# Kernel tuning notes

Hardware: AMD Instinct MI355X
Metric: run time of the kernel (lower is better)

The kernel has to match this reference:

```python
import jax, jax.numpy as jnp
import numpy as np

B, S, D, H, F, E, K = 2, 2048, 1024, 16, 4096, 8, 2
DH = D // H
EPS = 1e-6  # RMSNorm eps (torch nn.RMSNorm default ~ fp32 machine eps; 1e-6 used here)


def _rmsnorm(x, w):
    return x * jax.lax.rsqrt(jnp.mean(x * x, axis=-1, keepdims=True) + EPS) * w


def setup_inputs() -> dict:
    key = jax.random.key(0)
    ks = jax.random.split(key, 16)
    std = 0.02
    return {
        "x": jax.random.normal(ks[0], (B, S, D), jnp.float32),
        "norm1_w": jnp.ones((D,), jnp.float32),
        "norm2_w": jnp.ones((D,), jnp.float32),
        "w_qkv": jax.random.normal(ks[1], (D, 3 * D), jnp.float32) * std,
        "b_qkv": jnp.zeros((3 * D,), jnp.float32),
        "w_o": jax.random.normal(ks[2], (D, D), jnp.float32) * std,
        "b_o": jnp.zeros((D,), jnp.float32),
        "router_w": jax.random.normal(ks[3], (D, E), jnp.float32) * std,
        "router_b": jnp.zeros((E,), jnp.float32),
        "w1": jax.random.normal(ks[4], (E, D, F), jnp.float32) * std,
        "b1": jnp.zeros((E, F), jnp.float32),
        "w2": jax.random.normal(ks[5], (E, F, D), jnp.float32) * std,
        "b2": jnp.zeros((E, D), jnp.float32),
    }


def reference(x, norm1_w, norm2_w, w_qkv, b_qkv, w_o, b_o,
              router_w, router_b, w1, b1, w2, b2):
    # ---- pre-norm causal multi-head attention ----
    h = _rmsnorm(x, norm1_w)
    qkv = h @ w_qkv + b_qkv                                  # [B,S,3D]
    q, k, v = jnp.split(qkv, 3, axis=-1)
    q = q.reshape(B, S, H, DH).transpose(0, 2, 1, 3)         # [B,H,S,DH]
    k = k.reshape(B, S, H, DH).transpose(0, 2, 1, 3)
    v = v.reshape(B, S, H, DH).transpose(0, 2, 1, 3)
    scores = jnp.einsum('bhqd,bhkd->bhqk', q, k) / jnp.sqrt(jnp.asarray(DH, x.dtype))
    causal = jnp.tril(jnp.ones((S, S), bool))
    scores = jnp.where(causal, scores, jnp.asarray(-1e9, x.dtype))
    attn = jax.nn.softmax(scores, axis=-1)
    ao = jnp.einsum('bhqk,bhkd->bhqd', attn, v).transpose(0, 2, 1, 3).reshape(B, S, D)
    x = x + (ao @ w_o + b_o)

    # ---- pre-norm top-k MoE feed-forward ----
    h2 = _rmsnorm(x, norm2_w)
    t = h2.reshape(-1, D)                                    # [T,D], T=B*S
    logits = t @ router_w + router_b                         # [T,E]
    probs = jax.nn.softmax(logits, axis=-1)
    topv, topi = jax.lax.top_k(probs, K)                     # [T,K]
    gates_k = topv / jnp.sum(topv, axis=-1, keepdims=True)   # renormalized top-k gates
    oh = jax.nn.one_hot(topi, E, dtype=x.dtype)              # [T,K,E]
    gates = jnp.einsum('tke,tk->te', oh, gates_k)            # dense gates, zero off top-k

    out = jnp.zeros_like(t)
    for e in range(E):                                       # fixed small expert loop
        he = jax.nn.gelu(t @ w1[e] + b1[e], approximate=False)
        ye = he @ w2[e] + b2[e]
        out = out + gates[:, e:e + 1] * ye

    # load-balancing aux loss: E * sum_e f_e * P_e
    f = jnp.mean(jnp.sum(oh, axis=1), axis=0)                # fraction routed to each expert
    P = jnp.mean(probs, axis=0)                              # mean router prob per expert
    aux_loss = jnp.asarray(E, x.dtype) * jnp.sum(f * P)

    x = x + out.reshape(B, S, D)
    return (x, aux_loss)
```

## Files before the change

### kernel.cpp

```cpp
#include <hip/hip_runtime.h>
#include <math.h>

#define TB 2
#define TS 2048
#define TD 1024
#define TH 16
#define TDH 64
#define TF 4096
#define TE 8
#define TT 4096
#define PSTR (TB*TH*TS*TDH)

typedef __attribute__((ext_vector_type(8))) __bf16 bf16x8;
typedef __attribute__((ext_vector_type(4))) float f32x4;
typedef __attribute__((ext_vector_type(8))) short short8;
typedef __attribute__((ext_vector_type(4))) unsigned short ushort4v;
typedef __attribute__((ext_vector_type(4))) float fvec4;

__device__ inline unsigned short f2bf(float f) {
  union { float f; unsigned int u; } v; v.f = f;
  unsigned int u = v.u;
  unsigned int r = (u + 0x7FFFu + ((u >> 16) & 1u)) >> 16;
  return (unsigned short)r;
}
__device__ inline float bf2f(unsigned short h) {
  union { unsigned int u; float f; } v; v.u = ((unsigned int)h) << 16; return v.f;
}
__device__ inline void split2(float x, unsigned short& h, unsigned short& m) {
  h = f2bf(x);
  m = f2bf(x - bf2f(h));
}

__device__ inline f32x4 mfma_bf16(short8 a, short8 b, f32x4 c) {
  return __builtin_amdgcn_mfma_f32_16x16x32_bf16(
      __builtin_bit_cast(bf16x8, a), __builtin_bit_cast(bf16x8, b), c, 0, 0, 0);
}

__device__ inline void gload16(const void* g, void* l) {
  __builtin_amdgcn_global_load_lds(
      (const __attribute__((address_space(1))) void*)g,
      (__attribute__((address_space(3))) void*)l, 16, 0, 0);
}

__device__ inline float gelu_f(float v) {
  float ax = fabsf(v) * 0.70710678118654752f;
  float t = __builtin_amdgcn_rcpf(1.0f + 0.3275911f * ax);
  float poly = ((((1.061405429f * t - 1.453152027f) * t + 1.421413741f) * t
                 - 0.284496736f) * t + 0.254829592f) * t;
  float er = 1.0f - poly * __expf(-ax * ax);
  er = copysignf(er, v);
  return 0.5f * v * (1.0f + er);
}

__global__ __launch_bounds__(256)
void tcvt_kernel(const float* __restrict__ In, unsigned short* __restrict__ Out,
                 int R, int C) {
  __shared__ float tile[32][33];
  In  += (size_t)blockIdx.z * R * C;
  Out += (size_t)blockIdx.z * R * C;
  int c0 = blockIdx.x * 32, r0 = blockIdx.y * 32;
  int tx = threadIdx.x & 31, ty = threadIdx.x >> 5;
#pragma unroll
  for (int i = 0; i < 4; ++i)
    tile[ty + 8*i][tx] = In[(size_t)(r0 + ty + 8*i) * C + c0 + tx];
  __syncthreads();
#pragma unroll
  for (int i = 0; i < 4; ++i)
    Out[(size_t)(c0 + ty + 8*i) * R + r0 + tx] = f2bf(tile[tx][ty + 8*i]);
}

__global__ __launch_bounds__(256)
void tcvt_split_kernel(const float* __restrict__ In,
                       unsigned short* __restrict__ O0,
                       unsigned short* __restrict__ O1, int R, int C) {
  __shared__ float tile[32][33];
  int c0 = blockIdx.x * 32, r0 = blockIdx.y * 32;
  int tx = threadIdx.x & 31, ty = threadIdx.x >> 5;
#pragma unroll
  for (int i = 0; i < 4; ++i)
    tile[ty + 8*i][tx] = In[(size_t)(r0 + ty + 8*i) * C + c0 + tx];
  __syncthreads();
#pragma unroll
  for (int i = 0; i < 4; ++i) {
    float v = tile[tx][ty + 8*i];
    unsigned short h, m; split2(v, h, m);
    size_t idx = (size_t)(c0 + ty + 8*i) * R + r0 + tx;
    O0[idx] = h; O1[idx] = m;
  }
}

__global__ __launch_bounds__(256)
void rmsnorm_kernel(const float* __restrict__ X, const float* __restrict__ W,
                    unsigned short* __restrict__ O) {
  int row = blockIdx.x;
  int tid = threadIdx.x;
  int lane = tid & 63, wave = tid >> 6;
  const float* xr = X + (size_t)row * TD;
  fvec4 v = *(const fvec4*)(xr + tid * 4);
  float ss = v[0]*v[0] + v[1]*v[1] + v[2]*v[2] + v[3]*v[3];
#pragma unroll
  for (int msk = 1; msk < 64; msk <<= 1) ss += __shfl_xor(ss, msk);
  __shared__ float red[4];
  if (lane == 0) red[wave] = ss;
  __syncthreads();
  ss = red[0] + red[1] + red[2] + red[3];
  float rs = rsqrtf(ss * (1.0f / TD) + 1e-6f);
  fvec4 wv = *(const fvec4*)(W + tid * 4);
  ushort4v o;
#pragma unroll
  for (int j = 0; j < 4; ++j) o[j] = f2bf(v[j] * rs * wv[j]);
  *(ushort4v*)(O + (size_t)row * TD + tid * 4) = o;
}

__global__ __launch_bounds__(256)
void rmsnorm_split_kernel(const float* __restrict__ X, const float* __restrict__ W,
                          unsigned short* __restrict__ O0,
                          unsigned short* __restrict__ O1) {
  int row = blockIdx.x;
  int tid = threadIdx.x;
  int lane = tid & 63, wave = tid >> 6;
  const float* xr = X + (size_t)row * TD;
  fvec4 v = *(const fvec4*)(xr + tid * 4);
  float ss = v[0]*v[0] + v[1]*v[1] + v[2]*v[2] + v[3]*v[3];
#pragma unroll
  for (int msk = 1; msk < 64; msk <<= 1) ss += __shfl_xor(ss, msk);
  __shared__ float red[4];
  if (lane == 0) red[wave] = ss;
  __syncthreads();
  ss = red[0] + red[1] + red[2] + red[3];
  float rs = rsqrtf(ss * (1.0f / TD) + 1e-6f);
  fvec4 wv = *(const fvec4*)(W + tid * 4);
  ushort4v o0, o1;
#pragma unroll
  for (int j = 0; j < 4; ++j) {
    unsigned short h, m; split2(v[j] * rs * wv[j], h, m);
    o0[j] = h; o1[j] = m;
  }
  size_t idx = (size_t)row * TD + tid * 4;
  *(ushort4v*)(O0 + idx) = o0;
  *(ushort4v*)(O1 + idx) = o1;
}

template<int MODE>
__global__ __launch_bounds__(256)
void gemm2(const unsigned short* __restrict__ A0,
           const unsigned short* __restrict__ A1,
           const unsigned short* __restrict__ B0,
           const unsigned short* __restrict__ B1,
           const float* __restrict__ bias, int Kd,
           float* __restrict__ outF, const float* __restrict__ resid,
           unsigned short* __restrict__ S0,
           unsigned short* __restrict__ S1) {
  __shared__ __align__(16) unsigned short As0[2][4096], As1[2][4096];
  __shared__ __align__(16) unsigned short Bs0[2][4096], Bs1[2][4096];
  const int tid = threadIdx.x;
  const int lane = tid & 63;
  const int w = tid >> 6;
  const int wr = w >> 1, wc = w & 1;
  const int g = lane >> 4;
  const int l15 = lane & 15;
  const int m0 = blockIdx.y * 128;
  const int n0 = blockIdx.x * 128;

  const int c_swz = (lane & 3) ^ ((lane >> 3) & 3);
  const unsigned short *a0p[2], *a1p[2], *b0p[2], *b1p[2];
  int ldsrow[2];
#pragma unroll
  for (int j = 0; j < 2; ++j) {
    int r16 = w * 2 + j;
    int r = r16 * 16 + (lane >> 2);
    a0p[j] = A0 + (size_t)(m0 + r) * Kd + c_swz * 8;
    a1p[j] = A1 + (size_t)(m0 + r) * Kd + c_swz * 8;
    b0p[j] = B0 + (size_t)(n0 + r) * Kd + c_swz * 8;
    b1p[j] = B1 + (size_t)(n0 + r) * Kd + c_swz * 8;
    ldsrow[j] = r16 * 512;
  }

#define G2_STAGE(p, koff)                              \
  {                                                    \
    _Pragma("unroll")                                  \
    for (int j = 0; j < 2; ++j) {                      \
      gload16(a0p[j] + (koff), &As0[p][ldsrow[j]]);    \
      gload16(a1p[j] + (koff), &As1[p][ldsrow[j]]);    \
      gload16(b0p[j] + (koff), &Bs0[p][ldsrow[j]]);    \
      gload16(b1p[j] + (koff), &Bs1[p][ldsrow[j]]);    \
    }                                                  \
  }

  f32x4 acc[4][4] = {};
  const int nt = Kd >> 5;

  G2_STAGE(0, 0);
  for (int t = 0; t < nt; ++t) {
    const int p = t & 1;
    if (t + 1 < nt) {
      G2_STAGE(p ^ 1, (t + 1) * 32);
      asm volatile("s_waitcnt vmcnt(8)" ::: "memory");
    } else {
      asm volatile("s_waitcnt vmcnt(0)" ::: "memory");
    }
    __builtin_amdgcn_s_barrier();

    short8 a0f[4], a1f[4], b0f[4], b1f[4];
#pragma unroll
    for (int mi = 0; mi < 4; ++mi) {
      int row = wr * 64 + mi * 16 + l15;
      int off = (row * 64 + g * 16) ^ (((row >> 1) & 3) << 4);
      a0f[mi] = *(const short8*)((const char*)As0[p] + off);
      a1f[mi] = *(const short8*)((const char*)As1[p] + off);
    }
#pragma unroll
    for (int ni = 0; ni < 4; ++ni) {
      int row = wc * 64 + ni * 16 + l15;
      int off = (row * 64 + g * 16) ^ (((row >> 1) & 3) << 4);
      b0f[ni] = *(const short8*)((const char*)Bs0[p] + off);
      b1f[ni] = *(const short8*)((const char*)Bs1[p] + off);
    }
#pragma unroll
    for (int mi = 0; mi < 4; ++mi)
#pragma unroll
      for (int ni = 0; ni < 4; ++ni) {
        f32x4 tacc = acc[mi][ni];
        tacc = mfma_bf16(a0f[mi], b0f[ni], tacc);
        tacc = mfma_bf16(a0f[mi], b1f[ni], tacc);
        tacc = mfma_bf16(a1f[mi], b0f[ni], tacc);
        acc[mi][ni] = tacc;
      }
    __builtin_amdgcn_s_barrier();
  }
#undef G2_STAGE

#pragma unroll
  for (int mi = 0; mi < 4; ++mi) {
#pragma unroll
    for (int ni = 0; ni < 4; ++ni) {
      int n = n0 + wc * 64 + ni * 16 + l15;
      float bv = bias[n];
      if (MODE == 0) {
        int part = n >> 10, d = n & 1023, hh = d >> 6, dh = d & 63;
        int s0r = m0 + wr * 64 + mi * 16 + g * 4;
        int b = s0r >> 11, s_ = s0r & 2047;
        int bh = b * TH + hh;
        if (part < 2) {
          size_t base = (size_t)part * PSTR + (size_t)bh * (TS * TDH) + (size_t)s_ * TDH + dh;
#pragma unroll
          for (int r = 0; r < 4; ++r) {
            unsigned short h, m; split2(acc[mi][ni][r] + bv, h, m);
            size_t idx = base + (size_t)r * TDH;
            S0[idx] = h; S1[idx] = m;
          }
        } else {
          ushort4v o0, o1;
#pragma unroll
          for (int r = 0; r < 4; ++r) {
            unsigned short h, m; split2(acc[mi][ni][r] + bv, h, m);
            o0[r] = h; o1[r] = m;
          }
          size_t idx = 2 * (size_t)PSTR + (size_t)bh * (TS * TDH) + (size_t)dh * TS + s_;
          *(ushort4v*)(S0 + idx) = o0;
          *(ushort4v*)(S1 + idx) = o1;
        }
      } else {
#pragma unroll
        for (int r = 0; r < 4; ++r) {
          int m = m0 + wr * 64 + mi * 16 + g * 4 + r;
          size_t idx = (size_t)m * TD + n;
          outF[idx] = acc[mi][ni][r] + bv + resid[idx];
        }
      }
    }
  }
}

__global__ __launch_bounds__(512, 4)
void attn2_kernel(const unsigned short* __restrict__ S0,
                  const unsigned short* __restrict__ S1,
                  unsigned short* __restrict__ A0,
                  unsigned short* __restrict__ A1) {
  __shared__ __align__(16) char Kt0[8192], Kt1[8192];
  __shared__ __align__(16) char Vt0[8192], Vt1[8192];
  __shared__ __align__(16) char Pt0[16384], Pt1[16384];

  const int tid = threadIdx.x;
  const int lane = tid & 63;
  const int wave = tid >> 6;
  const int g = lane >> 4, l15 = lane & 15;

  const int bh = blockIdx.y;
  const int b = bh >> 4, hh = bh & 15;

  const size_t qbase = (size_t)bh * TS * TDH;
  const size_t kbase = (size_t)PSTR + qbase;
  const size_t vbase = 2 * (size_t)PSTR + qbase;

  for (int half = 0; half < 2; ++half) {
    const int qtb = half ? (15 - (int)blockIdx.x) : (int)blockIdx.x;
    const int qlo = qtb * 128 + wave * 16;

    short8 aq0[2], aq1[2];
#pragma unroll
    for (int c = 0; c < 2; ++c) {
      size_t qo = qbase + (size_t)(qlo + l15) * TDH + c * 32 + g * 8;
      aq0[c] = *(const short8*)(S0 + qo);
      aq1[c] = *(const short8*)(S1 + qo);
    }

    f32x4 accv[4] = {};
    float m_[4] = {-1e30f, -1e30f, -1e30f, -1e30f};
    float l_[4] = {0.f, 0.f, 0.f, 0.f};

    const int ktmax = 2 * qtb + 1;
    for (int kt = 0; kt <= ktmax; ++kt) {
      __syncthreads();
      {
        int row = tid >> 3, ch = tid & 7;
        int off = (row * 128 + ch * 16) ^ ((row & 7) << 4);
        size_t kg = kbase + (size_t)(kt * 64 + row) * TDH + ch * 8;
        *(short8*)(Kt0 + off) = *(const short8*)(S0 + kg);
        *(short8*)(Kt1 + off) = *(const short8*)(S1 + kg);
        size_t vg = vbase + (size_t)row * TS + kt * 64 + ch * 8;
        *(short8*)(Vt0 + off) = *(const short8*)(S0 + vg);
        *(short8*)(Vt1 + off) = *(const short8*)(S1 + vg);
      }
      __syncthreads();

      if (kt * 64 > qlo + 15) continue;
      const bool needmask = (kt * 64 + 63 > qlo);

      f32x4 sf[4] = {};
#pragma unroll
      for (int kb = 0; kb < 4; ++kb) {
#pragma unroll
        for (int c = 0; c < 2; ++c) {
          int krow = kb * 16 + l15;
          int off = (krow * 128 + (c * 32 + g * 8) * 2) ^ ((krow & 7) << 4);
          short8 bk0 = *(const short8*)(Kt0 + off);
          short8 bk1 = *(const short8*)(Kt1 + off);
          f32x4 t = sf[kb];
          t = mfma_bf16(aq0[c], bk0, t);
          t = mfma_bf16(aq0[c], bk1, t);
          t = mfma_bf16(aq1[c], bk0, t);
          sf[kb] = t;
        }
      }

      float pv[4][4];
#pragma unroll
      for (int r = 0; r < 4; ++r) {
        float s0 = sf[0][r] * 0.125f, s1 = sf[1][r] * 0.125f;
        float s2 = sf[2][r] * 0.125f, s3 = sf[3][r] * 0.125f;
        if (needmask) {
          int qg = qlo + g * 4 + r;
          int k0g = kt * 64 + l15;
          if (k0g      > qg) s0 = -1e30f;
          if (k0g + 16 > qg) s1 = -1e30f;
          if (k0g + 32 > qg) s2 = -1e30f;
          if (k0g + 48 > qg) s3 = -1e30f;
        }
        float mx = fmaxf(fmaxf(s0, s1), fmaxf(s2, s3));
#pragma unroll
        for (int msk = 1; msk < 16; msk <<= 1) mx = fmaxf(mx, __shfl_xor(mx, msk));
        float nm = fmaxf(m_[r], mx);
        float sc = __expf(m_[r] - nm);
        float p0 = __expf(s0 - nm), p1 = __expf(s1 - nm);
        float p2 = __expf(s2 - nm), p3 = __expf(s3 - nm);
        float rs = p0 + p1 + p2 + p3;
#pragma unroll
        for (int msk = 1; msk < 16; msk <<= 1) rs += __shfl_xor(rs, msk);
        m_[r] = nm;
        l_[r] = l_[r] * sc + rs;
#pragma unroll
        for (int dhb = 0; dhb < 4; ++dhb) accv[dhb][r] *= sc;
        pv[0][r] = p0; pv[1][r] = p1; pv[2][r] = p2; pv[3][r] = p3;
      }

      char* P0 = Pt0 + wave * 2048;
      char* P1 = Pt1 + wave * 2048;
#pragma unroll
      for (int kb = 0; kb < 4; ++kb) {
#pragma unroll
        for (int r = 0; r < 4; ++r) {
          int prow = g * 4 + r;
          int key = kb * 16 + l15;
          int off = (prow * 128 + key * 2) ^ ((prow & 7) << 4);
          unsigned short h, m; split2(pv[kb][r], h, m);
          *(unsigned short*)(P0 + off) = h;
          *(unsigned short*)(P1 + off) = m;
        }
      }
      short8 pa0[2], pa1[2];
#pragma unroll
      for (int c = 0; c < 2; ++c) {
        int off = (l15 * 128 + (c * 32 + g * 8) * 2) ^ ((l15 & 7) << 4);
        pa0[c] = *(const short8*)(P0 + off);
        pa1[c] = *(const short8*)(P1 + off);
      }
#pragma unroll
      for (int dhb = 0; dhb < 4; ++dhb) {
#pragma unroll
        for (int c = 0; c < 2; ++c) {
          int dh = dhb * 16 + l15;
          int off = (dh * 128 + (c * 32 + g * 8) * 2) ^ ((dh & 7) << 4);
          short8 bv0 = *(const short8*)(Vt0 + off);
          short8 bv1 = *(const short8*)(Vt1 + off);
          f32x4 t = accv[dhb];
          t = mfma_bf16(pa0[c], bv0, t);
          t = mfma_bf16(pa0[c], bv1, t);
          t = mfma_bf16(pa1[c], bv0, t);
          accv[dhb] = t;
        }
      }
    }

#pragma unroll
    for (int dhb = 0; dhb < 4; ++dhb) {
#pragma unroll
      for (int r = 0; r < 4; ++r) {
        int srow = qlo + g * 4 + r;
        int col = hh * 64 + dhb * 16 + l15;
        unsigned short h, m; split2(accv[dhb][r] / l_[r], h, m);
        size_t idx = ((size_t)(b * TS + srow)) * TD + col;
        A0[idx] = h; A1[idx] = m;
      }
    }
  }
}

__global__ __launch_bounds__(256)
void moe_gather_kernel(const unsigned short* __restrict__ h2,
                       const int* __restrict__ tperm,
                       unsigned short* __restrict__ h2p) {
  int slot = blockIdx.x;
  int t = tperm[slot];
  const ushort4v* src = (const ushort4v*)(h2 + (size_t)t * TD);
  ushort4v* dst = (ushort4v*)(h2p + (size_t)slot * TD);
  dst[threadIdx.x] = src[threadIdx.x];
}

__global__ __launch_bounds__(512)
void gemm_up8(const unsigned short* __restrict__ A,
              const unsigned short* __restrict__ Bt,
              const float* __restrict__ bias,
              int N, int Kd,
              unsigned short* __restrict__ outH,
              const int* __restrict__ seg_off,
              const int* __restrict__ seg_cnt) {
  __shared__ __align__(16) unsigned short As[2][256 * 64];
  __shared__ __align__(16) unsigned short Bs[2][256 * 64];

  const int tid = threadIdx.x;
  const int lane = tid & 63;
  const int w = tid >> 6;
  const int wm = w >> 2, wn = w & 3;
  const int g = lane >> 4;
  const int l15 = lane & 15;

  const int e = blockIdx.z;
  const int m0 = blockIdx.y * 256;
  const int n0 = blockIdx.x * 256;
  const int off = seg_off[e];
  const int Mrows = seg_cnt[e];
  if (m0 >= Mrows) return;
  Bt += (size_t)e * N * Kd;
  bias += (size_t)e * N;

  const int gc = (lane & 7) ^ ((lane >> 3) & 7);
  const unsigned short* aptr[4];
  const unsigned short* bptr[4];
#pragma unroll
  for (int rnd = 0; rnd < 4; ++rnd) {
    int rl = rnd * 64 + w * 8 + (lane >> 3);
    int rc = (m0 + rl < Mrows) ? (m0 + rl) : (Mrows - 1);
    aptr[rnd] = A + (size_t)(off + rc) * Kd + gc * 8;
    bptr[rnd] = Bt + (size_t)(n0 + rl) * Kd + gc * 8;
  }

#define UP8_STAGE(p, koff)                                        \
  {                                                               \
    _Pragma("unroll")                                             \
    for (int rnd = 0; rnd < 4; ++rnd) {                           \
      gload16(aptr[rnd] + (koff), &As[p][(rnd * 64 + w * 8) * 64]); \
      gload16(bptr[rnd] + (koff), &Bs[p][(rnd * 64 + w * 8) * 64]); \
    }                                                             \
  }

  f32x4 acc[8][4] = {};
  const int nt = Kd >> 6;

  UP8_STAGE(0, 0);
  __syncthreads();

  for (int t = 0; t < nt; ++t) {
    const int p = t & 1;
    if (t + 1 < nt) UP8_STAGE(p ^ 1, (t + 1) * 64);

#pragma unroll
    for (int ph = 0; ph < 4; ++ph) {
      const int mh = ph >> 1, kk = ph & 1;
      short8 af[4], bfr[4];
#pragma unroll
      for (int q = 0; q < 4; ++q) {
        int row = wm * 128 + (mh * 4 + q) * 16 + l15;
        int o2 = row * 128 + ((((kk << 2) | g) ^ (row & 7)) << 4);
        af[q] = *(const short8*)((const char*)As[p] + o2);
      }
#pragma unroll
      for (int ni = 0; ni < 4; ++ni) {
        int row = wn * 64 + ni * 16 + l15;
        int o2 = row * 128 + ((((kk << 2) | g) ^ (row & 7)) << 4);
        bfr[ni] = *(const short8*)((const char*)Bs[p] + o2);
      }
#pragma unroll
      for (int q = 0; q < 4; ++q)
#pragma unroll
        for (int ni = 0; ni < 4; ++ni)
          acc[mh * 4 + q][ni] = mfma_bf16(af[q], bfr[ni], acc[mh * 4 + q][ni]);
    }
    __syncthreads();
  }
#undef UP8_STAGE

#pragma unroll
  for (int mi = 0; mi < 8; ++mi) {
#pragma unroll
    for (int ni = 0; ni < 4; ++ni) {
      int n = n0 + wn * 64 + ni * 16 + l15;
      float bv = bias[n];
#pragma unroll
      for (int r = 0; r < 4; ++r) {
        int mloc = m0 + wm * 128 + mi * 16 + g * 4 + r;
        if (mloc >= Mrows) continue;
        float val = acc[mi][ni][r] + bv;
        outH[(size_t)(off + mloc) * TF + n] = f2bf(gelu_f(val));
      }
    }
  }
}

__global__ __launch_bounds__(256)
void gemm_dn(const unsigned short* __restrict__ A,
             const unsigned short* __restrict__ Bt,
             const float* __restrict__ bias,
             int N, int Kd,
             float* __restrict__ ysl,
             const int* __restrict__ seg_off,
             const int* __restrict__ seg_cnt,
             const float* __restrict__ gate_perm) {
  __shared__ __align__(16) unsigned short As[2][4096];
  __shared__ __align__(16) unsigned short Bs[2][4096];

  const int tid = threadIdx.x;
  const int lane = tid & 63;
  const int w = tid >> 6;
  const int wr = w >> 1, wc = w & 1;
  const int g = lane >> 4;
  const int l15 = lane & 15;

  const int e = blockIdx.z;
  const int m0 = blockIdx.y * 128;
  const int n0 = blockIdx.x * 128;
  const int off = seg_off[e];
  const int Mrows = seg_cnt[e];
  if (m0 >= Mrows) return;
  Bt += (size_t)e * N * Kd;
  bias += (size_t)e * N;

  const int c_swz = (lane & 3) ^ ((lane >> 3) & 3);
  const unsigned short* aptr[2];
  const unsigned short* bptr[2];
  int ldsrow[2];
#pragma unroll
  for (int j = 0; j < 2; ++j) {
    int r16 = w * 2 + j;
    int r = r16 * 16 + (lane >> 2);
    int rc = (m0 + r < Mrows) ? (m0 + r) : (Mrows - 1);
    aptr[j] = A + (size_t)(off + rc) * Kd + c_swz * 8;
    bptr[j] = Bt + (size_t)(n0 + r) * Kd + c_swz * 8;
    ldsrow[j] = r16 * 512;
  }

#define GB_STAGE(p, koff)                           \
  {                                                 \
    _Pragma("unroll")                               \
    for (int j = 0; j < 2; ++j) {                   \
      gload16(aptr[j] + (koff), &As[p][ldsrow[j]]); \
      gload16(bptr[j] + (koff), &Bs[p][ldsrow[j]]); \
    }                                               \
  }

  f32x4 acc[4][4] = {};
  const int nt = Kd >> 5;

  GB_STAGE(0, 0);
  for (int t = 0; t < nt; ++t) {
    const int p = t & 1;
    if (t + 1 < nt) {
      GB_STAGE(p ^ 1, (t + 1) * 32);
      asm volatile("s_waitcnt vmcnt(4)" ::: "memory");
    } else {
      asm volatile("s_waitcnt vmcnt(0)" ::: "memory");
    }
    __builtin_amdgcn_s_barrier();

    short8 af[4], bfr[4];
#pragma unroll
    for (int mi = 0; mi < 4; ++mi) {
      int row = wr * 64 + mi * 16 + l15;
      int o2 = (row * 64 + g * 16) ^ (((row >> 1) & 3) << 4);
      af[mi] = *(const short8*)((const char*)As[p] + o2);
    }
#pragma unroll
    for (int ni = 0; ni < 4; ++ni) {
      int row = wc * 64 + ni * 16 + l15;
      int o2 = (row * 64 + g * 16) ^ (((row >> 1) & 3) << 4);
      bfr[ni] = *(const short8*)((const char*)Bs[p] + o2);
    }
#pragma unroll
    for (int mi = 0; mi < 4; ++mi)
#pragma unroll
      for (int ni = 0; ni < 4; ++ni)
        acc[mi][ni] = mfma_bf16(af[mi], bfr[ni], acc[mi][ni]);
    __builtin_amdgcn_s_barrier();
  }
#undef GB_STAGE

#pragma unroll
  for (int mi = 0; mi < 4; ++mi) {
#pragma unroll
    for (int ni = 0; ni < 4; ++ni) {
      int n = n0 + wc * 64 + ni * 16 + l15;
      float bv = bias[n];
#pragma unroll
      for (int r = 0; r < 4; ++r) {
        int mloc = m0 + wr * 64 + mi * 16 + g * 4 + r;
        if (mloc >= Mrows) continue;
        float val = acc[mi][ni][r] + bv;
        float gv = gate_perm[off + mloc];
        ysl[(size_t)(off + mloc) * TD + n] = gv * val;
      }
    }
  }
}

__global__ __launch_bounds__(256)
void moe_reduce_kernel(const float* __restrict__ ys, const int* __restrict__ tslot,
                       float* __restrict__ out) {
  int t = blockIdx.x;
  int d = threadIdx.x * 4;
  fvec4 a = *(const fvec4*)(ys + (size_t)tslot[t * 2] * TD + d);
  fvec4 b = *(const fvec4*)(ys + (size_t)tslot[t * 2 + 1] * TD + d);
  float* o = out + (size_t)t * TD + d;
  fvec4 c = *(const fvec4*)o;
#pragma unroll
  for (int j = 0; j < 4; ++j) c[j] += a[j] + b[j];
  *(fvec4*)o = c;
}

__global__ __launch_bounds__(256)
void router_kernel(const float* __restrict__ X1, const float* __restrict__ N2W,
                   const float* __restrict__ RW, const float* __restrict__ RB,
                   int* __restrict__ top_e, float* __restrict__ top_g,
                   int* __restrict__ counts, float* __restrict__ p_sum) {
  __shared__ float s_psum[TE];
  __shared__ int s_cnt[TE];
  if (threadIdx.x < TE) { s_psum[threadIdx.x] = 0.f; s_cnt[threadIdx.x] = 0; }
  __syncthreads();
  int lane = threadIdx.x & 63, wave = threadIdx.x >> 6;
  for (int it = 0; it < 16; ++it) {
    int t = (blockIdx.x * 4 + wave) * 16 + it;
    const float* xr = X1 + (size_t)t * TD;
    float vals[16]; float ss = 0.f;
#pragma unroll
    for (int i = 0; i < 16; ++i) { float xv = xr[i * 64 + lane]; vals[i] = xv; ss += xv * xv; }
#pragma unroll
    for (int msk = 1; msk < 64; msk <<= 1) ss += __shfl_xor(ss, msk);
    float rs = rsqrtf(ss * (1.0f / TD) + 1e-6f);
    float acc[TE] = {};
#pragma unroll
    for (int i = 0; i < 16; ++i) {
      int d = i * 64 + lane;
      float nv = vals[i] * rs * N2W[d];
      const float* rwp = RW + (size_t)d * TE;
#pragma unroll
      for (int e2 = 0; e2 < TE; ++e2) acc[e2] += nv * rwp[e2];
    }
#pragma unroll
    for (int msk = 1; msk < 64; msk <<= 1)
#pragma unroll
      for (int e2 = 0; e2 < TE; ++e2) acc[e2] += __shfl_xor(acc[e2], msk);
    if (lane == 0) {
      float lg[TE]; float mx = -1e30f;
      for (int e2 = 0; e2 < TE; ++e2) { lg[e2] = acc[e2] + RB[e2]; mx = fmaxf(mx, lg[e2]); }
      float sum = 0.f, pe[TE];
      for (int e2 = 0; e2 < TE; ++e2) { pe[e2] = expf(lg[e2] - mx); sum += pe[e2]; }
      float inv = 1.0f / sum;
      for (int e2 = 0; e2 < TE; ++e2) atomicAdd(&s_psum[e2], pe[e2] * inv);
      int i1 = 0;
      for (int e2 = 1; e2 < TE; ++e2) if (lg[e2] > lg[i1]) i1 = e2;
      int i2 = (i1 == 0) ? 1 : 0;
      for (int e2 = 0; e2 < TE; ++e2) if (e2 != i1 && lg[e2] > lg[i2]) i2 = e2;
      float g1 = pe[i1], g2 = pe[i2], gs = g1 + g2;
      top_e[t * 2] = i1; top_e[t * 2 + 1] = i2;
      top_g[t * 2] = g1 / gs; top_g[t * 2 + 1] = g2 / gs;
      atomicAdd(&s_cnt[i1], 1); atomicAdd(&s_cnt[i2], 1);
    }
  }
  __syncthreads();
  if (threadIdx.x < TE) {
    atomicAdd(&p_sum[threadIdx.x], s_psum[threadIdx.x]);
    atomicAdd(&counts[threadIdx.x], s_cnt[threadIdx.x]);
  }
}

__global__ void zero_meta_kernel(int* counts, float* p_sum) {
  int t = threadIdx.x;
  if (t < TE) { counts[t] = 0; p_sum[t] = 0.f; }
}

__global__ void offsets_kernel(const int* counts, int* offs, int* cursor) {
  if (threadIdx.x == 0) {
    int o = 0;
    for (int e2 = 0; e2 < TE; ++e2) { offs[e2] = o; o += counts[e2]; }
  }
  if (threadIdx.x < TE) cursor[threadIdx.x] = 0;
}

__global__ __launch_bounds__(256)
void fill_kernel(const int* __restrict__ top_e, const float* __restrict__ top_g,
                 const int* __restrict__ offs, int* __restrict__ cursor,
                 int* __restrict__ token_perm, float* __restrict__ gate_perm,
                 int* __restrict__ tslot) {
  __shared__ int s_cnt[TE], s_base[TE];
  if (threadIdx.x < TE) s_cnt[threadIdx.x] = 0;
  __syncthreads();
  int t = blockIdx.x * 256 + threadIdx.x;
  int e0 = top_e[t * 2], e1 = top_e[t * 2 + 1];
  int r0 = atomicAdd(&s_cnt[e0], 1);
  int r1 = atomicAdd(&s_cnt[e1], 1);
  __syncthreads();
  if (threadIdx.x < TE)
    s_base[threadIdx.x] = atomicAdd(&cursor[threadIdx.x], s_cnt[threadIdx.x]);
  __syncthreads();
  int p0 = offs[e0] + s_base[e0] + r0;
  int p1 = offs[e1] + s_base[e1] + r1;
  token_perm[p0] = t; gate_perm[p0] = top_g[t * 2];
  token_perm[p1] = t; gate_perm[p1] = top_g[t * 2 + 1];
  tslot[t * 2] = p0; tslot[t * 2 + 1] = p1;
}

__global__ void aux_kernel(const int* counts, const float* p_sum, float* outv) {
  if (threadIdx.x == 0) {
    float a = 0.f;
    for (int e2 = 0; e2 < TE; ++e2)
      a += ((float)counts[e2] / (float)TT) * (p_sum[e2] / (float)TT);
    outv[0] = (float)TE * a;
  }
}

extern "C" void kernel_launch(void* const* d_in, const int* in_sizes, int n_in,
                              void* d_out, int out_size, void* d_ws, size_t ws_size,
                              hipStream_t stream) {
  const float* x     = (const float*)d_in[0];
  const float* n1w   = (const float*)d_in[1];
  const float* n2w   = (const float*)d_in[2];
  const float* w_qkv = (const float*)d_in[3];
  const float* b_qkv = (const float*)d_in[4];
  const float* w_o   = (const float*)d_in[5];
  const float* b_o   = (const float*)d_in[6];
  const float* rw    = (const float*)d_in[7];
  const float* rb    = (const float*)d_in[8];
  const float* w1    = (const float*)d_in[9];
  const float* b1    = (const float*)d_in[10];
  const float* w2    = (const float*)d_in[11];
  const float* b2    = (const float*)d_in[12];
  float* out = (float*)d_out;
  char* ws = (char*)d_ws;

  size_t o = 0;
  auto give = [&](size_t bytes) -> char* {
    char* p = ws + o;
    o += (bytes + 255) & ~(size_t)255;
    return p;
  };
  unsigned short* w1T = (unsigned short*)give(8ull * 4096 * 1024 * 2);
  unsigned short* w2T = (unsigned short*)give(8ull * 1024 * 4096 * 2);
  unsigned short* wo0 = (unsigned short*)give(1024ull * 1024 * 2);
  unsigned short* wo1 = (unsigned short*)give(1024ull * 1024 * 2);
  unsigned short* h2  = (unsigned short*)give((size_t)TT * TD * 2);
  int*   counts = (int*)give(TE * 4);
  int*   cursor = (int*)give(TE * 4);
  int*   offs   = (int*)give(TE * 4);
  float* psum   = (float*)give(TE * 4);
  int*   top_e  = (int*)give(2ull * TT * 4);
  float* top_g  = (float*)give(2ull * TT * 4);
  int*   tperm  = (int*)give(2ull * TT * 4);
  float* gperm  = (float*)give(2ull * TT * 4);
  int*   tslot  = (int*)give(2ull * TT * 4);
  unsigned short* wq0 = (unsigned short*)give(3072ull * 1024 * 2);
  unsigned short* wq1 = (unsigned short*)give(3072ull * 1024 * 2);
  float* ys = (float*)give(2ull * TT * TD * 4);
  char* poolB = give(2ull * TT * TD * 2);
  unsigned short* h10 = (unsigned short*)poolB;
  unsigned short* h11 = (unsigned short*)(poolB + (size_t)TT * TD * 2);
  unsigned short* ao0 = h10; unsigned short* ao1 = h11;
  unsigned short* h2p = (unsigned short*)poolB;
  char* poolC = give(64ull * 1024 * 1024);
  unsigned short* qs0 = (unsigned short*)poolC;
  unsigned short* qs1 = (unsigned short*)(poolC + 3ull * PSTR * 2);
  unsigned short* he  = (unsigned short*)poolC;

  tcvt_split_kernel<<<dim3(96, 32, 1), 256, 0, stream>>>(w_qkv, wq0, wq1, 1024, 3072);
  tcvt_split_kernel<<<dim3(32, 32, 1), 256, 0, stream>>>(w_o, wo0, wo1, 1024, 1024);
  tcvt_kernel<<<dim3(128, 32, 8), 256, 0, stream>>>(w1, w1T, 1024, 4096);
  tcvt_kernel<<<dim3(32, 128, 8), 256, 0, stream>>>(w2, w2T, 4096, 1024);

  rmsnorm_split_kernel<<<dim3(TT), 256, 0, stream>>>(x, n1w, h10, h11);
  gemm2<0><<<dim3(24, 32, 1), 256, 0, stream>>>(
      h10, h11, wq0, wq1, b_qkv, 1024, nullptr, nullptr, qs0, qs1);
  attn2_kernel<<<dim3(8, 32, 1), 512, 0, stream>>>(qs0, qs1, ao0, ao1);
  gemm2<1><<<dim3(8, 32, 1), 256, 0, stream>>>(
      ao0, ao1, wo0, wo1, b_o, 1024, out, x, nullptr, nullptr);

  rmsnorm_kernel<<<dim3(TT), 256, 0, stream>>>(out, n2w, h2);
  zero_meta_kernel<<<dim3(1), 64, 0, stream>>>(counts, psum);
  router_kernel<<<dim3(64), 256, 0, stream>>>(out, n2w, rw, rb, top_e, top_g, counts, psum);
  offsets_kernel<<<dim3(1), 64, 0, stream>>>(counts, offs, cursor);
  fill_kernel<<<dim3(TT / 256), 256, 0, stream>>>(top_e, top_g, offs, cursor, tperm, gperm, tslot);
  moe_gather_kernel<<<dim3(2 * TT), 256, 0, stream>>>(h2, tperm, h2p);
  gemm_up8<<<dim3(16, 16, 8), 512, 0, stream>>>(
      h2p, w1T, b1, 4096, 1024, he, offs, counts);
  gemm_dn<<<dim3(8, 32, 8), 256, 0, stream>>>(
      he, w2T, b2, 1024, 4096, ys, offs, counts, gperm);
  moe_reduce_kernel<<<dim3(TT), 256, 0, stream>>>(ys, tslot, out);
  aux_kernel<<<dim3(1), 64, 0, stream>>>(counts, psum, out + (size_t)TT * TD);
}
```

Baseline: 756.9 us.

## Enlarge MoE down-proj GEMM tile to 256x128 with K=64 stages and counted waits

Replaces the 128x128, K=32 down-projection GEMM with a 512-thread, 256x128-tile kernel that uses K=64 stages and an XOR-swizzled LDS layout taken from the up-projection kernel. The larger tile halves the number of blocks and re-reads each B tile fewer times. It also swaps the up-projection kernel's __syncthreads for an explicit vmcnt wait plus barrier, so the prefetch for the next stage stays in flight during compute. In exchange it uses more LDS per block, and a single block covers more padded rows for small expert segments.

Result: slower. 828.2 us (+9.4%).

```diff
diff --git a/kernel.cpp b/kernel.cpp
--- a/kernel.cpp
+++ b/kernel.cpp
@@ -488,11 +488,15 @@
   const int nt = Kd >> 6;
 
   UP8_STAGE(0, 0);
-  __syncthreads();
-
   for (int t = 0; t < nt; ++t) {
     const int p = t & 1;
-    if (t + 1 < nt) UP8_STAGE(p ^ 1, (t + 1) * 64);
+    if (t + 1 < nt) {
+      UP8_STAGE(p ^ 1, (t + 1) * 64);
+      asm volatile("s_waitcnt vmcnt(8)" ::: "memory");
+    } else {
+      asm volatile("s_waitcnt vmcnt(0)" ::: "memory");
+    }
+    __builtin_amdgcn_s_barrier();
 
 #pragma unroll
     for (int ph = 0; ph < 4; ++ph) {
@@ -516,7 +520,7 @@
         for (int ni = 0; ni < 4; ++ni)
           acc[mh * 4 + q][ni] = mfma_bf16(af[q], bfr[ni], acc[mh * 4 + q][ni]);
     }
-    __syncthreads();
+    __builtin_amdgcn_s_barrier();
   }
 #undef UP8_STAGE
 
@@ -537,27 +541,27 @@
   }
 }
 
-__global__ __launch_bounds__(256)
-void gemm_dn(const unsigned short* __restrict__ A,
-             const unsigned short* __restrict__ Bt,
-             const float* __restrict__ bias,
-             int N, int Kd,
-             float* __restrict__ ysl,
-             const int* __restrict__ seg_off,
-             const int* __restrict__ seg_cnt,
-             const float* __restrict__ gate_perm) {
-  __shared__ __align__(16) unsigned short As[2][4096];
-  __shared__ __align__(16) unsigned short Bs[2][4096];
+__global__ __launch_bounds__(512)
+void gemm_dn8(const unsigned short* __restrict__ A,
+              const unsigned short* __restrict__ Bt,
+              const float* __restrict__ bias,
+              int N, int Kd,
+              float* __restrict__ ysl,
+              const int* __restrict__ seg_off,
+              const int* __restrict__ seg_cnt,
+              const float* __restrict__ gate_perm) {
+  __shared__ __align__(16) unsigned short As[2][256 * 64];
+  __shared__ __align__(16) unsigned short Bs[2][128 * 64];
 
   const int tid = threadIdx.x;
   const int lane = tid & 63;
   const int w = tid >> 6;
-  const int wr = w >> 1, wc = w & 1;
+  const int wm = w >> 1, wn = w & 1;
   const int g = lane >> 4;
   const int l15 = lane & 15;
 
   const int e = blockIdx.z;
-  const int m0 = blockIdx.y * 128;
+  const int m0 = blockIdx.y * 256;
   const int n0 = blockIdx.x * 128;
   const int off = seg_off[e];
   const int Mrows = seg_cnt[e];
@@ -565,74 +569,79 @@
   Bt += (size_t)e * N * Kd;
   bias += (size_t)e * N;
 
-  const int c_swz = (lane & 3) ^ ((lane >> 3) & 3);
-  const unsigned short* aptr[2];
+  const int gc = (lane & 7) ^ ((lane >> 3) & 7);
+  const unsigned short* aptr[4];
   const unsigned short* bptr[2];
-  int ldsrow[2];
+#pragma unroll
+  for (int rnd = 0; rnd < 4; ++rnd) {
+    int rl = rnd * 64 + w * 8 + (lane >> 3);
+    int rc = (m0 + rl < Mrows) ? (m0 + rl) : (Mrows - 1);
+    aptr[rnd] = A + (size_t)(off + rc) * Kd + gc * 8;
+  }
 #pragma unroll
   for (int j = 0; j < 2; ++j) {
-    int r16 = w * 2 + j;
-    int r = r16 * 16 + (lane >> 2);
-    int rc = (m0 + r < Mrows) ? (m0 + r) : (Mrows - 1);
-    aptr[j] = A + (size_t)(off + rc) * Kd + c_swz * 8;
-    bptr[j] = Bt + (size_t)(n0 + r) * Kd + c_swz * 8;
-    ldsrow[j] = r16 * 512;
-  }
-
-#define GB_STAGE(p, koff)                           \
-  {                                                 \
-    _Pragma("unroll")                               \
-    for (int j = 0; j < 2; ++j) {                   \
-      gload16(aptr[j] + (koff), &As[p][ldsrow[j]]); \
-      gload16(bptr[j] + (koff), &Bs[p][ldsrow[j]]); \
-    }                                               \
+    int rl = w * 16 + j * 8 + (lane >> 3);
+    bptr[j] = Bt + (size_t)(n0 + rl) * Kd + gc * 8;
+  }
+
+#define DN8_STAGE(p, koff)                                          \
+  {                                                                 \
+    _Pragma("unroll")                                               \
+    for (int rnd = 0; rnd < 4; ++rnd)                               \
+      gload16(aptr[rnd] + (koff), &As[p][(rnd * 64 + w * 8) * 64]); \
+    _Pragma("unroll")                                               \
+    for (int j = 0; j < 2; ++j)                                     \
+      gload16(bptr[j] + (koff), &Bs[p][(w * 16 + j * 8) * 64]);     \
   }
 
   f32x4 acc[4][4] = {};
-  const int nt = Kd >> 5;
-
-  GB_STAGE(0, 0);
+  const int nt = Kd >> 6;
+
+  DN8_STAGE(0, 0);
   for (int t = 0; t < nt; ++t) {
     const int p = t & 1;
     if (t + 1 < nt) {
-      GB_STAGE(p ^ 1, (t + 1) * 32);
-      asm volatile("s_waitcnt vmcnt(4)" ::: "memory");
+      DN8_STAGE(p ^ 1, (t + 1) * 64);
+      asm volatile("s_waitcnt vmcnt(6)" ::: "memory");
     } else {
       asm volatile("s_waitcnt vmcnt(0)" ::: "memory");
     }
     __builtin_amdgcn_s_barrier();
 
-    short8 af[4], bfr[4];
-#pragma unroll
-    for (int mi = 0; mi < 4; ++mi) {
-      int row = wr * 64 + mi * 16 + l15;
-      int o2 = (row * 64 + g * 16) ^ (((row >> 1) & 3) << 4);
-      af[mi] = *(const short8*)((const char*)As[p] + o2);
-    }
+#pragma unroll
+    for (int kk = 0; kk < 2; ++kk) {
+      short8 af[4], bfr[4];
+#pragma unroll
+      for (int mi = 0; mi < 4; ++mi) {
+        int row = wm * 64 + mi * 16 + l15;
+        int o2 = row * 128 + ((((kk << 2) | g) ^ (row & 7)) << 4);
+        af[mi] = *(const short8*)((const char*)As[p] + o2);
+      }
+#pragma unroll
+      for (int ni = 0; ni < 4; ++ni) {
+        int row = wn * 64 + ni * 16 + l15;
+        int o2 = row * 128 + ((((kk << 2) | g) ^ (row & 7)) << 4);
+        bfr[ni] = *(const short8*)((const char*)Bs[p] + o2);
+      }
+#pragma unroll
+      for (int mi = 0; mi < 4; ++mi)
+#pragma unroll
+        for (int ni = 0; ni < 4; ++ni)
+          acc[mi][ni] = mfma_bf16(af[mi], bfr[ni], acc[mi][ni]);
+    }
+    __builtin_amdgcn_s_barrier();
+  }
+#undef DN8_STAGE
+
+#pragma unroll
+  for (int mi = 0; mi < 4; ++mi) {
 #pragma unroll
     for (int ni = 0; ni < 4; ++ni) {
-      int row = wc * 64 + ni * 16 + l15;
-      int o2 = (row * 64 + g * 16) ^ (((row >> 1) & 3) << 4);
-      bfr[ni] = *(const short8*)((const char*)Bs[p] + o2);
-    }
-#pragma unroll
-    for (int mi = 0; mi < 4; ++mi)
-#pragma unroll
-      for (int ni = 0; ni < 4; ++ni)
-        acc[mi][ni] = mfma_bf16(af[mi], bfr[ni], acc[mi][ni]);
-    __builtin_amdgcn_s_barrier();
-  }
-#undef GB_STAGE
-
-#pragma unroll
-  for (int mi = 0; mi < 4; ++mi) {
-#pragma unroll
-    for (int ni = 0; ni < 4; ++ni) {
-      int n = n0 + wc * 64 + ni * 16 + l15;
+      int n = n0 + wn * 64 + ni * 16 + l15;
       float bv = bias[n];
 #pragma unroll
       for (int r = 0; r < 4; ++r) {
-        int mloc = m0 + wr * 64 + mi * 16 + g * 4 + r;
+        int mloc = m0 + wm * 64 + mi * 16 + g * 4 + r;
         if (mloc >= Mrows) continue;
         float val = acc[mi][ni][r] + bv;
         float gv = gate_perm[off + mloc];
@@ -829,7 +838,7 @@
   moe_gather_kernel<<<dim3(2 * TT), 256, 0, stream>>>(h2, tperm, h2p);
   gemm_up8<<<dim3(16, 16, 8), 512, 0, stream>>>(
       h2p, w1T, b1, 4096, 1024, he, offs, counts);
-  gemm_dn<<<dim3(8, 32, 8), 256, 0, stream>>>(
+  gemm_dn8<<<dim3(8, 16, 8), 512, 0, stream>>>(
       he, w2T, b2, 1024, 4096, ys, offs, counts, gperm);
   moe_reduce_kernel<<<dim3(TT), 256, 0, stream>>>(ys, tslot, out);
   aux_kernel<<<dim3(1), 64, 0, stream>>>(counts, psum, out + (size_t)TT * TD);
```
